# Kernel tuning notes

Measured on AMD Instinct MI355X. Metric: run time of the kernel, lower is better.

## Reference

```python
import jax, jax.numpy as jnp
import numpy as np

B, T, C = 2, 2048, 1024
H = 16
DK = C // H


def setup_inputs() -> dict:
    key = jax.random.key(0)
    ks = jax.random.split(key, 5)
    x = jax.random.normal(ks[0], (B, T, C), dtype=jnp.float32)
    # causal mask, broadcastable to [B, H, T, T]; mask==0 -> -inf
    mask = jnp.tril(jnp.ones((T, T), dtype=jnp.int32))[None, None]
    s = 1.0 / np.sqrt(C)
    qkv_w = jax.random.normal(ks[1], (3 * C, C), dtype=jnp.float32) * s  # torch Linear layout [out,in]
    qkv_b = jnp.zeros((3 * C,), dtype=jnp.float32)
    out_w = jax.random.normal(ks[2], (C, C), dtype=jnp.float32) * s
    out_b = jnp.zeros((C,), dtype=jnp.float32)
    return {"x": x, "mask": mask, "qkv_w": qkv_w, "qkv_b": qkv_b,
            "out_w": out_w, "out_b": out_b}


def reference(x, mask, qkv_w, qkv_b, out_w, out_b):
    b, t, c = x.shape
    qkv = x @ qkv_w.T + qkv_b                       # [B,T,3C]
    qkv = qkv.reshape(b, t, 3, H, DK)
    q, k, v = qkv[:, :, 0], qkv[:, :, 1], qkv[:, :, 2]   # [B,T,H,DK]
    scores = jnp.einsum('bqhd,bkhd->bhqk', q, k) / np.sqrt(DK)
    scores = jnp.where(mask == 0, -jnp.inf, scores)
    attn_weights = jax.nn.softmax(scores, axis=-1)       # [B,H,T,T]
    attn_out = jnp.einsum('bhqk,bkhd->bqhd', attn_weights, v).reshape(b, t, c)
    out = attn_out @ out_w.T + out_b
    return out, attn_weights
```

## Files before the change

kernel.cpp:

```cpp
#include <hip/hip_runtime.h>
#include <hip/hip_bf16.h>

typedef short short8  __attribute__((ext_vector_type(8)));
typedef short short4v __attribute__((ext_vector_type(4)));
typedef __bf16 bf16x8 __attribute__((ext_vector_type(8)));
typedef float f32x4   __attribute__((ext_vector_type(4)));

__device__ __forceinline__ void mfma16(f32x4& d, short8 a, short8 b) {
    d = __builtin_amdgcn_mfma_f32_16x16x32_bf16(
            __builtin_bit_cast(bf16x8, a), __builtin_bit_cast(bf16x8, b), d, 0, 0, 0);
}

__device__ __forceinline__ unsigned short f2bf(float f) {
    union { float f; unsigned u; } a; a.f = f;
    unsigned u = a.u;
    return (unsigned short)((u + 0x7fffu + ((u >> 16) & 1u)) >> 16);
}
__device__ __forceinline__ float bf2f(unsigned short us) {
    union { unsigned u; float f; } a; a.u = ((unsigned)us) << 16;
    return a.f;
}

__global__ void cvt_all(const float* __restrict__ x, const float* __restrict__ w1,
                        const float* __restrict__ w2,
                        unsigned short* __restrict__ ox, unsigned short* __restrict__ o1,
                        unsigned short* __restrict__ o2) {
    int i = blockIdx.x * 256 + threadIdx.x;
    const float* src; unsigned short* dst; int j;
    if (i < 1048576)      { src = x;  dst = ox; j = i; }
    else if (i < 1835008) { src = w1; dst = o1; j = i - 1048576; }
    else                  { src = w2; dst = o2; j = i - 1835008; }
    float4 v = ((const float4*)src)[j];
    ushort4 o;
    o.x = f2bf(v.x); o.y = f2bf(v.y); o.z = f2bf(v.z); o.w = f2bf(v.w);
    ((ushort4*)dst)[j] = o;
}

template<int OUTBF, int VTF>
__global__ __launch_bounds__(256)
void gemm_bt(const unsigned short* __restrict__ A, const unsigned short* __restrict__ Bw,
             const float* __restrict__ bias, void* __restrict__ Cout,
             unsigned short* __restrict__ vt, int M, int N, int K)
{
    __shared__ unsigned short As[128 * 64];
    __shared__ unsigned short Bs[128 * 64];

    const int tid  = threadIdx.x;
    const int lane = tid & 63;
    const int wid  = tid >> 6;
    const int swz  = (int)((blockIdx.x & 7) * (gridDim.x >> 3) + (blockIdx.x >> 3));
    const int nby  = M >> 7;
    const int row0 = (swz % nby) << 7;
    const int col0 = (swz / nby) << 7;
    const int wr = (wid >> 1) << 6;
    const int wc = (wid & 1) << 6;
    const int rl = lane & 15;
    const int g  = lane >> 4;

    f32x4 acc[4][4] = {};

    for (int k0 = 0; k0 < K; k0 += 64) {
        __syncthreads();
#pragma unroll
        for (int rd = 0; rd < 4; ++rd) {
            int s  = rd * 256 + tid;
            int r  = s >> 3, cs = s & 7;
            int cg = cs ^ (r & 7);
            __builtin_amdgcn_global_load_lds(
                (__attribute__((address_space(1))) void*)(A + (size_t)(row0 + r) * K + k0 + cg * 8),
                (__attribute__((address_space(3))) void*)(As + s * 8), 16, 0, 0);
            __builtin_amdgcn_global_load_lds(
                (__attribute__((address_space(1))) void*)(Bw + (size_t)(col0 + r) * K + k0 + cg * 8),
                (__attribute__((address_space(3))) void*)(Bs + s * 8), 16, 0, 0);
        }
        __syncthreads();

#pragma unroll
        for (int h = 0; h < 2; ++h) {
            short8 af[4], bf[4];
#pragma unroll
            for (int m = 0; m < 4; ++m) {
                int rr = wr + m * 16 + rl;
                int ch = ((h << 2) + g) ^ (rr & 7);
                af[m] = *(const short8*)(As + rr * 64 + ch * 8);
            }
#pragma unroll
            for (int n = 0; n < 4; ++n) {
                int rr = wc + n * 16 + rl;
                int ch = ((h << 2) + g) ^ (rr & 7);
                bf[n] = *(const short8*)(Bs + rr * 64 + ch * 8);
            }
#pragma unroll
            for (int m = 0; m < 4; ++m)
#pragma unroll
                for (int n = 0; n < 4; ++n)
                    mfma16(acc[m][n], af[m], bf[n]);
        }
    }

    const int b  = row0 >> 11;
    const int tg = (row0 & 2047) + wr + (g << 2);
#pragma unroll
    for (int n = 0; n < 4; ++n) {
        int col = col0 + wc + n * 16 + rl;
        float bv = bias[col];
        if (VTF && col >= 2048) {
            int hd = col - 2048;
            unsigned short* vr = vt + ((size_t)((b << 4) + (hd >> 6)) * 64 + (hd & 63)) * 2048;
#pragma unroll
            for (int m = 0; m < 4; ++m) {
                short4v p;
#pragma unroll
                for (int r = 0; r < 4; ++r) p[r] = (short)f2bf(acc[m][n][r] + bv);
                *(short4v*)(vr + tg + m * 16) = p;
            }
        } else {
#pragma unroll
            for (int m = 0; m < 4; ++m) {
#pragma unroll
                for (int r = 0; r < 4; ++r) {
                    int row = row0 + wr + m * 16 + (g << 2) + r;
                    float v = acc[m][n][r] + bv;
                    if (OUTBF) ((unsigned short*)Cout)[(size_t)row * N + col] = f2bf(v);
                    else       __builtin_nontemporal_store(v, (float*)Cout + (size_t)row * N + col);
                }
            }
        }
    }
}

__device__ __forceinline__ int S_addr(int row, int col) {
    return (row << 11) + ((((col >> 3) ^ (row & 7))) << 3) + (col & 7);
}

__global__ __launch_bounds__(256, 2)
void attn_kernel(const unsigned short* __restrict__ qkv,
                 const unsigned short* __restrict__ vt,
                 float* __restrict__ wout,
                 unsigned short* __restrict__ aout)
{
    __shared__ unsigned short Ss[16 * 2048];
    __shared__ float part[4][16];

    const int bid = (int)(((blockIdx.x & 7) << 9) + (blockIdx.x >> 3));
    const int qt = bid & 127;
    const int bh = bid >> 7;
    const int b = bh >> 4, h = bh & 15;
    const int q0 = qt << 4;
    const int tid = threadIdx.x;
    const int wid = tid >> 6;
    const int lane = tid & 63;
    const int rl = lane & 15;
    const int g  = lane >> 4;

    int nt = (qt + 4) & ~3;
    if (nt > 128) nt = 128;
    const int ntiles = nt;
    const int KPAD = ntiles << 4;

    const unsigned short* Qb = qkv + (size_t)((b << 11) + q0) * 3072 + (h << 6);
    short8 qf0 = *(const short8*)(Qb + (size_t)rl * 3072 + g * 8);
    short8 qf1 = *(const short8*)(Qb + (size_t)rl * 3072 + 32 + g * 8);

    const unsigned short* Kb = qkv + (size_t)(b << 11) * 3072 + 1024 + (h << 6);

    float psum[4] = {0.f, 0.f, 0.f, 0.f};

    {
        int kt = wid;
        const unsigned short* kp = Kb + (size_t)(kt * 16 + rl) * 3072;
        short8 ka0 = *(const short8*)(kp + g * 8);
        short8 ka1 = *(const short8*)(kp + 32 + g * 8);
        for (; kt < ntiles; kt += 4) {
            short8 kb0 = ka0, kb1 = ka1;
            if (kt + 4 < ntiles) {
                const unsigned short* kp2 = Kb + (size_t)((kt + 4) * 16 + rl) * 3072;
                kb0 = *(const short8*)(kp2 + g * 8);
                kb1 = *(const short8*)(kp2 + 32 + g * 8);
            }
            f32x4 acc = {};
            __builtin_amdgcn_s_setprio(1);
            mfma16(acc, qf0, ka0);
            mfma16(acc, qf1, ka1);
            __builtin_amdgcn_s_setprio(0);
            int col = kt * 16 + rl;
#pragma unroll
            for (int r = 0; r < 4; ++r) {
                int qrow = g * 4 + r;
                float e = (col <= q0 + qrow) ? __expf(acc[r] * 0.125f) : 0.0f;
                Ss[S_addr(qrow, col)] = f2bf(e);
                psum[r] += e;
            }
            ka0 = kb0; ka1 = kb1;
        }
    }
#pragma unroll
    for (int m = 8; m; m >>= 1)
#pragma unroll
        for (int r = 0; r < 4; ++r) psum[r] += __shfl_xor(psum[r], m);
    if (rl == 0) {
#pragma unroll
        for (int r = 0; r < 4; ++r) part[wid][g * 4 + r] = psum[r];
    }
    __syncthreads();

    for (int r = wid; r < 16; r += 4) {
        float inv = 1.0f / (part[0][r] + part[1][r] + part[2][r] + part[3][r]);
        float* orow = wout + ((size_t)bh * 2048 + q0 + r) * 2048;
        for (int j8 = lane * 8; j8 < KPAD; j8 += 512) {
            short8 ev = *(const short8*)(Ss + S_addr(r, j8));
            f32x4 o0, o1;
            o0[0] = bf2f((unsigned short)ev[0]) * inv;
            o0[1] = bf2f((unsigned short)ev[1]) * inv;
            o0[2] = bf2f((unsigned short)ev[2]) * inv;
            o0[3] = bf2f((unsigned short)ev[3]) * inv;
            o1[0] = bf2f((unsigned short)ev[4]) * inv;
            o1[1] = bf2f((unsigned short)ev[5]) * inv;
            o1[2] = bf2f((unsigned short)ev[6]) * inv;
            o1[3] = bf2f((unsigned short)ev[7]) * inv;
            __builtin_nontemporal_store(o0, (f32x4*)(orow + j8));
            __builtin_nontemporal_store(o1, (f32x4*)(orow + j8 + 4));
        }
        f32x4 z = {0.f, 0.f, 0.f, 0.f};
        for (int j = KPAD + (lane << 2); j < 2048; j += 256)
            __builtin_nontemporal_store(z, (f32x4*)(orow + j));
    }

    f32x4 p0 = {}, p1 = {};
    const unsigned short* vrow = vt + ((size_t)(bh << 6) + wid * 16 + rl) * 2048;
    const int nkc = KPAD >> 5;
    for (int kc = 0; kc < nkc; kc += 2) {
        int c0 = (kc << 2) + g;
        short8 a0 = *(const short8*)(Ss + (rl << 11) + ((c0 ^ (rl & 7)) << 3));
        short8 b0 = *(const short8*)(vrow + (kc << 5) + (g << 3));
        int c1 = c0 + 4;
        short8 a1 = *(const short8*)(Ss + (rl << 11) + ((c1 ^ (rl & 7)) << 3));
        short8 b1 = *(const short8*)(vrow + ((kc + 1) << 5) + (g << 3));
        __builtin_amdgcn_s_setprio(1);
        mfma16(p0, a0, b0);
        mfma16(p1, a1, b1);
        __builtin_amdgcn_s_setprio(0);
    }
    f32x4 pacc = p0 + p1;
#pragma unroll
    for (int r = 0; r < 4; ++r) {
        int qrow = g * 4 + r;
        float inv = 1.0f / (part[0][qrow] + part[1][qrow] + part[2][qrow] + part[3][qrow]);
        float v = pacc[r] * inv;
        aout[(size_t)((b << 11) + q0 + qrow) * 1024 + (h << 6) + wid * 16 + rl] = f2bf(v);
    }
}

extern "C" void kernel_launch(void* const* d_in, const int* in_sizes, int n_in,
                              void* d_out, int out_size, void* d_ws, size_t ws_size,
                              hipStream_t stream)
{
    const float* x     = (const float*)d_in[0];
    const float* qkv_w = (const float*)d_in[2];
    const float* qkv_b = (const float*)d_in[3];
    const float* out_w = (const float*)d_in[4];
    const float* out_b = (const float*)d_in[5];

    char* ws = (char*)d_ws;
    unsigned short* xbf   = (unsigned short*)(ws);
    unsigned short* wqkv  = (unsigned short*)(ws + 8388608);
    unsigned short* woutw = (unsigned short*)(ws + 14680064);
    unsigned short* qkv   = (unsigned short*)(ws + 16777216);
    unsigned short* vt    = (unsigned short*)(ws + 41943040);
    unsigned short* aout  = (unsigned short*)(ws + 50331648);

    float* out  = (float*)d_out;
    float* wout = (float*)d_out + 4194304;

    cvt_all<<<8192, 256, 0, stream>>>(x, qkv_w, out_w, xbf, wqkv, woutw);

    gemm_bt<1, 1><<<768, 256, 0, stream>>>(xbf, wqkv, qkv_b, qkv, vt, 4096, 3072, 1024);
    attn_kernel<<<4096, 256, 0, stream>>>(qkv, vt, wout, aout);
    gemm_bt<0, 0><<<256, 256, 0, stream>>>(aout, woutw, out_b, out, nullptr, 4096, 1024, 1024);
}
```

Measured before the change: 234.0 us.

## Move causal-mask zero fill into QKV GEMM blocks and narrow output GEMM tiles

```diff
diff --git a/kernel.cpp b/kernel.cpp
--- a/kernel.cpp
+++ b/kernel.cpp
@@ -36,28 +36,55 @@
     ((ushort4*)dst)[j] = o;
 }
 
-template<int OUTBF, int VTF>
+template<int OUTBF, int VTF, int BN, int ZF>
 __global__ __launch_bounds__(256)
 void gemm_bt(const unsigned short* __restrict__ A, const unsigned short* __restrict__ Bw,
              const float* __restrict__ bias, void* __restrict__ Cout,
-             unsigned short* __restrict__ vt, int M, int N, int K)
+             unsigned short* __restrict__ vt, float* __restrict__ zwout,
+             int M, int N, int K)
 {
+    constexpr int NN = BN / 32;
     __shared__ unsigned short As[128 * 64];
-    __shared__ unsigned short Bs[128 * 64];
+    __shared__ unsigned short Bs[BN * 64];
 
     const int tid  = threadIdx.x;
     const int lane = tid & 63;
     const int wid  = tid >> 6;
-    const int swz  = (int)((blockIdx.x & 7) * (gridDim.x >> 3) + (blockIdx.x >> 3));
+
+    int gid;
+    if constexpr (ZF) {
+        if (((blockIdx.x >> 3) & 3) == 3) {
+            const int zid = ((blockIdx.x >> 5) << 3) + (blockIdx.x & 7);
+            f32x4 z = {0.f, 0.f, 0.f, 0.f};
+            for (int i = 0; i < 62; ++i) {
+                int tau = zid + (i << 8);
+                int bh = tau / 496, s = tau - bh * 496;
+                int c0 = (int)((sqrtf(8.f * (float)s + 1.f) - 1.f) * 0.5f);
+                while ((c0 + 1) * (c0 + 2) / 2 <= s) ++c0;
+                while (c0 * (c0 + 1) / 2 > s) --c0;
+                int ct = c0 + 1, qc = s - c0 * (c0 + 1) / 2;
+                int qrow = (qc << 6) + (tid >> 2);
+                float* dst = zwout + ((size_t)bh * 2048 + qrow) * 2048 + (ct << 6) + ((tid & 3) << 4);
+#pragma unroll
+                for (int u = 0; u < 4; ++u) __builtin_nontemporal_store(z, (f32x4*)dst + u);
+            }
+            return;
+        }
+        gid = (blockIdx.x >> 5) * 24 + (((blockIdx.x >> 3) & 3) << 3) + (blockIdx.x & 7);
+    } else {
+        gid = (int)blockIdx.x;
+    }
+    const int nblk = ZF ? 768 : (int)gridDim.x;
+    const int swz  = (gid & 7) * (nblk >> 3) + (gid >> 3);
     const int nby  = M >> 7;
     const int row0 = (swz % nby) << 7;
-    const int col0 = (swz / nby) << 7;
+    const int col0 = (swz / nby) * BN;
     const int wr = (wid >> 1) << 6;
-    const int wc = (wid & 1) << 6;
+    const int wc = (wid & 1) * (BN >> 1);
     const int rl = lane & 15;
     const int g  = lane >> 4;
 
-    f32x4 acc[4][4] = {};
+    f32x4 acc[4][NN] = {};
 
     for (int k0 = 0; k0 < K; k0 += 64) {
         __syncthreads();
@@ -69,6 +96,12 @@
             __builtin_amdgcn_global_load_lds(
                 (__attribute__((address_space(1))) void*)(A + (size_t)(row0 + r) * K + k0 + cg * 8),
                 (__attribute__((address_space(3))) void*)(As + s * 8), 16, 0, 0);
+        }
+#pragma unroll
+        for (int rd = 0; rd < (BN >> 5); ++rd) {
+            int s  = rd * 256 + tid;
+            int r  = s >> 3, cs = s & 7;
+            int cg = cs ^ (r & 7);
             __builtin_amdgcn_global_load_lds(
                 (__attribute__((address_space(1))) void*)(Bw + (size_t)(col0 + r) * K + k0 + cg * 8),
                 (__attribute__((address_space(3))) void*)(Bs + s * 8), 16, 0, 0);
@@ -77,7 +110,7 @@
 
 #pragma unroll
         for (int h = 0; h < 2; ++h) {
-            short8 af[4], bf[4];
+            short8 af[4], bf[NN];
 #pragma unroll
             for (int m = 0; m < 4; ++m) {
                 int rr = wr + m * 16 + rl;
@@ -85,7 +118,7 @@
                 af[m] = *(const short8*)(As + rr * 64 + ch * 8);
             }
 #pragma unroll
-            for (int n = 0; n < 4; ++n) {
+            for (int n = 0; n < NN; ++n) {
                 int rr = wc + n * 16 + rl;
                 int ch = ((h << 2) + g) ^ (rr & 7);
                 bf[n] = *(const short8*)(Bs + rr * 64 + ch * 8);
@@ -93,7 +126,7 @@
 #pragma unroll
             for (int m = 0; m < 4; ++m)
 #pragma unroll
-                for (int n = 0; n < 4; ++n)
+                for (int n = 0; n < NN; ++n)
                     mfma16(acc[m][n], af[m], bf[n]);
         }
     }
@@ -101,7 +134,7 @@
     const int b  = row0 >> 11;
     const int tg = (row0 & 2047) + wr + (g << 2);
 #pragma unroll
-    for (int n = 0; n < 4; ++n) {
+    for (int n = 0; n < NN; ++n) {
         int col = col0 + wc + n * 16 + rl;
         float bv = bias[col];
         if (VTF && col >= 2048) {
@@ -221,9 +254,6 @@
             __builtin_nontemporal_store(o0, (f32x4*)(orow + j8));
             __builtin_nontemporal_store(o1, (f32x4*)(orow + j8 + 4));
         }
-        f32x4 z = {0.f, 0.f, 0.f, 0.f};
-        for (int j = KPAD + (lane << 2); j < 2048; j += 256)
-            __builtin_nontemporal_store(z, (f32x4*)(orow + j));
     }
 
     f32x4 p0 = {}, p1 = {};
@@ -274,7 +304,7 @@
 
     cvt_all<<<8192, 256, 0, stream>>>(x, qkv_w, out_w, xbf, wqkv, woutw);
 
-    gemm_bt<1, 1><<<768, 256, 0, stream>>>(xbf, wqkv, qkv_b, qkv, vt, 4096, 3072, 1024);
+    gemm_bt<1, 1, 128, 1><<<1024, 256, 0, stream>>>(xbf, wqkv, qkv_b, qkv, vt, wout, 4096, 3072, 1024);
     attn_kernel<<<4096, 256, 0, stream>>>(qkv, vt, wout, aout);
-    gemm_bt<0, 0><<<256, 256, 0, stream>>>(aout, woutw, out_b, out, nullptr, 4096, 1024, 1024);
-}
+    gemm_bt<0, 0, 64, 0><<<512, 256, 0, stream>>>(aout, woutw, out_b, out, nullptr, nullptr, 4096, 1024, 1024);
+}
```

New measurement: 387.7 us. +65.7%, slower.

## Interleave attention-weight stores with PV MFMA loop and narrow output GEMM tile

Applied to the files above, without the earlier changes.

```diff
diff --git a/kernel.cpp b/kernel.cpp
--- a/kernel.cpp
+++ b/kernel.cpp
@@ -5,6 +5,7 @@
 typedef short short4v __attribute__((ext_vector_type(4)));
 typedef __bf16 bf16x8 __attribute__((ext_vector_type(8)));
 typedef float f32x4   __attribute__((ext_vector_type(4)));
+typedef float f32x2   __attribute__((ext_vector_type(2)));
 
 __device__ __forceinline__ void mfma16(f32x4& d, short8 a, short8 b) {
     d = __builtin_amdgcn_mfma_f32_16x16x32_bf16(
@@ -36,28 +37,30 @@
     ((ushort4*)dst)[j] = o;
 }
 
-template<int OUTBF, int VTF>
+template<int OUTBF, int VTF, int BN>
 __global__ __launch_bounds__(256)
 void gemm_bt(const unsigned short* __restrict__ A, const unsigned short* __restrict__ Bw,
              const float* __restrict__ bias, void* __restrict__ Cout,
              unsigned short* __restrict__ vt, int M, int N, int K)
 {
+    constexpr int NN = BN / 32;
     __shared__ unsigned short As[128 * 64];
-    __shared__ unsigned short Bs[128 * 64];
+    __shared__ unsigned short Bs[BN * 64];
 
     const int tid  = threadIdx.x;
     const int lane = tid & 63;
     const int wid  = tid >> 6;
+
     const int swz  = (int)((blockIdx.x & 7) * (gridDim.x >> 3) + (blockIdx.x >> 3));
     const int nby  = M >> 7;
     const int row0 = (swz % nby) << 7;
-    const int col0 = (swz / nby) << 7;
+    const int col0 = (swz / nby) * BN;
     const int wr = (wid >> 1) << 6;
-    const int wc = (wid & 1) << 6;
+    const int wc = (wid & 1) * (BN >> 1);
     const int rl = lane & 15;
     const int g  = lane >> 4;
 
-    f32x4 acc[4][4] = {};
+    f32x4 acc[4][NN] = {};
 
     for (int k0 = 0; k0 < K; k0 += 64) {
         __syncthreads();
@@ -69,6 +72,12 @@
             __builtin_amdgcn_global_load_lds(
                 (__attribute__((address_space(1))) void*)(A + (size_t)(row0 + r) * K + k0 + cg * 8),
                 (__attribute__((address_space(3))) void*)(As + s * 8), 16, 0, 0);
+        }
+#pragma unroll
+        for (int rd = 0; rd < (BN >> 5); ++rd) {
+            int s  = rd * 256 + tid;
+            int r  = s >> 3, cs = s & 7;
+            int cg = cs ^ (r & 7);
             __builtin_amdgcn_global_load_lds(
                 (__attribute__((address_space(1))) void*)(Bw + (size_t)(col0 + r) * K + k0 + cg * 8),
                 (__attribute__((address_space(3))) void*)(Bs + s * 8), 16, 0, 0);
@@ -77,7 +86,7 @@
 
 #pragma unroll
         for (int h = 0; h < 2; ++h) {
-            short8 af[4], bf[4];
+            short8 af[4], bf[NN];
 #pragma unroll
             for (int m = 0; m < 4; ++m) {
                 int rr = wr + m * 16 + rl;
@@ -85,7 +94,7 @@
                 af[m] = *(const short8*)(As + rr * 64 + ch * 8);
             }
 #pragma unroll
-            for (int n = 0; n < 4; ++n) {
+            for (int n = 0; n < NN; ++n) {
                 int rr = wc + n * 16 + rl;
                 int ch = ((h << 2) + g) ^ (rr & 7);
                 bf[n] = *(const short8*)(Bs + rr * 64 + ch * 8);
@@ -93,7 +102,7 @@
 #pragma unroll
             for (int m = 0; m < 4; ++m)
 #pragma unroll
-                for (int n = 0; n < 4; ++n)
+                for (int n = 0; n < NN; ++n)
                     mfma16(acc[m][n], af[m], bf[n]);
         }
     }
@@ -101,7 +110,7 @@
     const int b  = row0 >> 11;
     const int tg = (row0 & 2047) + wr + (g << 2);
 #pragma unroll
-    for (int n = 0; n < 4; ++n) {
+    for (int n = 0; n < NN; ++n) {
         int col = col0 + wc + n * 16 + rl;
         float bv = bias[col];
         if (VTF && col >= 2048) {
@@ -204,43 +213,34 @@
     }
     __syncthreads();
 
-    for (int r = wid; r < 16; r += 4) {
-        float inv = 1.0f / (part[0][r] + part[1][r] + part[2][r] + part[3][r]);
-        float* orow = wout + ((size_t)bh * 2048 + q0 + r) * 2048;
-        for (int j8 = lane * 8; j8 < KPAD; j8 += 512) {
-            short8 ev = *(const short8*)(Ss + S_addr(r, j8));
-            f32x4 o0, o1;
-            o0[0] = bf2f((unsigned short)ev[0]) * inv;
-            o0[1] = bf2f((unsigned short)ev[1]) * inv;
-            o0[2] = bf2f((unsigned short)ev[2]) * inv;
-            o0[3] = bf2f((unsigned short)ev[3]) * inv;
-            o1[0] = bf2f((unsigned short)ev[4]) * inv;
-            o1[1] = bf2f((unsigned short)ev[5]) * inv;
-            o1[2] = bf2f((unsigned short)ev[6]) * inv;
-            o1[3] = bf2f((unsigned short)ev[7]) * inv;
-            __builtin_nontemporal_store(o0, (f32x4*)(orow + j8));
-            __builtin_nontemporal_store(o1, (f32x4*)(orow + j8 + 4));
-        }
-        f32x4 z = {0.f, 0.f, 0.f, 0.f};
-        for (int j = KPAD + (lane << 2); j < 2048; j += 256)
-            __builtin_nontemporal_store(z, (f32x4*)(orow + j));
-    }
-
     f32x4 p0 = {}, p1 = {};
     const unsigned short* vrow = vt + ((size_t)(bh << 6) + wid * 16 + rl) * 2048;
     const int nkc = KPAD >> 5;
-    for (int kc = 0; kc < nkc; kc += 2) {
-        int c0 = (kc << 2) + g;
-        short8 a0 = *(const short8*)(Ss + (rl << 11) + ((c0 ^ (rl & 7)) << 3));
-        short8 b0 = *(const short8*)(vrow + (kc << 5) + (g << 3));
-        int c1 = c0 + 4;
-        short8 a1 = *(const short8*)(Ss + (rl << 11) + ((c1 ^ (rl & 7)) << 3));
-        short8 b1 = *(const short8*)(vrow + ((kc + 1) << 5) + (g << 3));
-        __builtin_amdgcn_s_setprio(1);
-        mfma16(p0, a0, b0);
-        mfma16(p1, a1, b1);
-        __builtin_amdgcn_s_setprio(0);
-    }
+    const int wrow = wid + (g << 2);
+    const float invw = 1.0f / (part[0][wrow] + part[1][wrow] + part[2][wrow] + part[3][wrow]);
+    float* worow = wout + ((size_t)bh * 2048 + q0 + wrow) * 2048;
+    const int cb = rl << 1;
+    short8 bv = *(const short8*)(vrow + (g << 3));
+    for (int ic = 0; ic < 64; ++ic) {
+        int colb = (ic << 5) + cb;
+        f32x2 o;
+        if (ic < nkc) {
+            short8 bcur = bv;
+            if (ic + 1 < nkc) bv = *(const short8*)(vrow + ((ic + 1) << 5) + (g << 3));
+            int c0 = (ic << 2) + g;
+            short8 a0 = *(const short8*)(Ss + (rl << 11) + ((c0 ^ (rl & 7)) << 3));
+            __builtin_amdgcn_s_setprio(1);
+            if (ic & 1) mfma16(p1, a0, bcur); else mfma16(p0, a0, bcur);
+            __builtin_amdgcn_s_setprio(0);
+            unsigned sv = *(const unsigned*)(Ss + S_addr(wrow, colb));
+            o[0] = bf2f((unsigned short)(sv & 0xffffu)) * invw;
+            o[1] = bf2f((unsigned short)(sv >> 16)) * invw;
+        } else {
+            o[0] = 0.f; o[1] = 0.f;
+        }
+        __builtin_nontemporal_store(o, (f32x2*)(worow + colb));
+    }
+
     f32x4 pacc = p0 + p1;
 #pragma unroll
     for (int r = 0; r < 4; ++r) {
@@ -274,7 +274,7 @@
 
     cvt_all<<<8192, 256, 0, stream>>>(x, qkv_w, out_w, xbf, wqkv, woutw);
 
-    gemm_bt<1, 1><<<768, 256, 0, stream>>>(xbf, wqkv, qkv_b, qkv, vt, 4096, 3072, 1024);
+    gemm_bt<1, 1, 128><<<768, 256, 0, stream>>>(xbf, wqkv, qkv_b, qkv, vt, 4096, 3072, 1024);
     attn_kernel<<<4096, 256, 0, stream>>>(qkv, vt, wout, aout);
-    gemm_bt<0, 0><<<256, 256, 0, stream>>>(aout, woutw, out_b, out, nullptr, 4096, 1024, 1024);
-}
+    gemm_bt<0, 0, 64><<<512, 256, 0, stream>>>(aout, woutw, out_b, out, nullptr, 4096, 1024, 1024);
+}
```

Measured after the change: 237.2 us. No clear change (+1.4%).
